# Kernel tuning notes

Measured on AMD Instinct MI355X. Metric: run time of the kernel, lower is better.

The kernel has to match this reference:

```python
import jax, jax.numpy as jnp
import numpy as np

HIDDEN = 4096
N_HEADS = 32
N_KV_HEADS = 2
HEAD_DIM = 128          # hidden // n_heads
ROT_DIM = HEAD_DIM // 2  # partial rotary (ChatGLM style)
ROPE_THETA = 10000.0
Q_SIZE = N_HEADS * HEAD_DIM
KV_SIZE = N_KV_HEADS * HEAD_DIM
SCALE = HEAD_DIM ** -0.5
T = 2048


def setup_inputs() -> dict:
    key = jax.random.key(0)
    k1, k2, k3, k4 = jax.random.split(key, 4)
    hidden_states = jax.random.normal(k1, (T, HIDDEN), dtype=jnp.float32)
    positions = jnp.arange(T, dtype=jnp.int64) if jax.config.jax_enable_x64 else jnp.arange(T, dtype=jnp.int32)
    w_qkv = jax.random.normal(k2, (Q_SIZE + 2 * KV_SIZE, HIDDEN), dtype=jnp.float32) * 0.02
    b_qkv = jax.random.normal(k3, (Q_SIZE + 2 * KV_SIZE,), dtype=jnp.float32) * 0.02
    w_dense = jax.random.normal(k4, (HIDDEN, Q_SIZE), dtype=jnp.float32) * 0.02
    return {"hidden_states": hidden_states, "positions": positions,
            "w_qkv": w_qkv, "b_qkv": b_qkv, "w_dense": w_dense}


def _apply_rope(x, positions):
    # x: [T, H, HEAD_DIM]; interleaved (is_neox_style=False) partial rotary on first ROT_DIM dims
    half = ROT_DIM // 2
    inv_freq = 1.0 / (ROPE_THETA ** (jnp.arange(0, half, dtype=jnp.float32) * 2.0 / ROT_DIM))
    freqs = positions.astype(jnp.float32)[:, None] * inv_freq[None, :]   # [T, half]
    cos = jnp.cos(freqs)[:, None, :]  # [T, 1, half]
    sin = jnp.sin(freqs)[:, None, :]
    x_rot = x[..., :ROT_DIM]
    x_pass = x[..., ROT_DIM:]
    x1 = x_rot[..., 0::2]
    x2 = x_rot[..., 1::2]
    o1 = x1 * cos - x2 * sin
    o2 = x2 * cos + x1 * sin
    rot = jnp.stack([o1, o2], axis=-1).reshape(x_rot.shape)  # re-interleave
    return jnp.concatenate([rot, x_pass], axis=-1)


def reference(hidden_states, positions, w_qkv, b_qkv, w_dense):
    # QKV projection (bias from add_qkv_bias=True)
    qkv = hidden_states @ w_qkv.T + b_qkv                     # [T, 4608]
    q = qkv[:, :Q_SIZE].reshape(T, N_HEADS, HEAD_DIM)
    k = qkv[:, Q_SIZE:Q_SIZE + KV_SIZE].reshape(T, N_KV_HEADS, HEAD_DIM)
    v = qkv[:, Q_SIZE + KV_SIZE:].reshape(T, N_KV_HEADS, HEAD_DIM)

    q = _apply_rope(q, positions)
    k = _apply_rope(k, positions)

    # GQA: expand 2 kv heads -> 32 q heads (each kv head serves 16 q heads)
    rep = N_HEADS // N_KV_HEADS
    k = jnp.repeat(k, rep, axis=1)                            # [T, 32, 128]
    v = jnp.repeat(v, rep, axis=1)

    # Causal scaled dot-product attention
    scores = jnp.einsum('thd,shd->hts', q, k) * SCALE         # [H, T, T]
    causal = positions[:, None] >= positions[None, :]          # [T, T]
    scores = jnp.where(causal[None, :, :], scores, jnp.finfo(scores.dtype).min)
    probs = jax.nn.softmax(scores, axis=-1)
    attn = jnp.einsum('hts,shd->thd', probs, v).reshape(T, Q_SIZE)

    # Output projection (no bias: add_bias_linear=False)
    return attn @ w_dense.T
```

## Files before the change

### kernel.cpp

```cpp
#include <hip/hip_runtime.h>
#include <cstdint>
#include <math.h>

typedef __bf16 bf16;
typedef __bf16 bf16x8 __attribute__((ext_vector_type(8)));
typedef __bf16 bf16x4 __attribute__((ext_vector_type(4)));
typedef float f32x4 __attribute__((ext_vector_type(4)));

#define T_SEQ 2048
#define HID   4096
#define NQH   32
#define NKVH  2
#define HD    128
#define NQKV  4608
#define ATT_SCALE 0.08838834764831845f

__device__ __forceinline__ void load_lds16(const void* g, void* l) {
    auto gp = (const __attribute__((address_space(1))) unsigned int*)(uintptr_t)g;
    auto lp = (__attribute__((address_space(3))) unsigned int*)(unsigned int)(uintptr_t)l;
    __builtin_amdgcn_global_load_lds(gp, lp, 16, 0, 0);
}

__device__ __forceinline__ f32x4 mfma16(bf16x8 a, bf16x8 b, f32x4 c) {
    return __builtin_amdgcn_mfma_f32_16x16x32_bf16(a, b, c, 0, 0, 0);
}

__global__ void cvt_f32_bf16_kernel(const float* __restrict__ x, bf16* __restrict__ y) {
    size_t i = ((size_t)blockIdx.x * 256 + threadIdx.x) * 8;
    float4 a = *(const float4*)(x + i);
    float4 b = *(const float4*)(x + i + 4);
    bf16x8 o;
    o[0] = (bf16)a.x; o[1] = (bf16)a.y; o[2] = (bf16)a.z; o[3] = (bf16)a.w;
    o[4] = (bf16)b.x; o[5] = (bf16)b.y; o[6] = (bf16)b.z; o[7] = (bf16)b.w;
    *(bf16x8*)(y + i) = o;
}

template <int OUT_BF16, int HAS_BIAS>
__global__ __launch_bounds__(256) void gemm_bt(const bf16* __restrict__ A,
                                               const bf16* __restrict__ B,
                                               const float* __restrict__ bias,
                                               void* __restrict__ Cout,
                                               int M, int N, int K) {
    __shared__ __align__(16) char sA[16384];
    __shared__ __align__(16) char sB[16384];
    const int tid = threadIdx.x;
    const int wid = tid >> 6, l = tid & 63, l4 = l >> 4, l16 = l & 15;
    const int wm = wid >> 1, wn = wid & 1;
    const int bm = blockIdx.x * 128, bn = blockIdx.y * 128;

    f32x4 acc[4][4] = {};

    const int c = tid;
    const int row0 = c >> 3, cc0 = c & 7;

    for (int k0 = 0; k0 < K; k0 += 64) {
        __syncthreads();
#pragma unroll
        for (int c4 = 0; c4 < 4; ++c4) {
            int ch = c4 * 256 + tid;
            int row = ch >> 3, cch = ch & 7;
            int scc = cch ^ (row & 7);
            load_lds16(A + (size_t)(bm + row) * K + k0 + scc * 8,
                       sA + c4 * 4096 + wid * 1024);
        }
#pragma unroll
        for (int c4 = 0; c4 < 4; ++c4) {
            int ch = c4 * 256 + tid;
            int row = ch >> 3, cch = ch & 7;
            int scc = cch ^ (row & 7);
            load_lds16(B + (size_t)(bn + row) * K + k0 + scc * 8,
                       sB + c4 * 4096 + wid * 1024);
        }
        __syncthreads();
#pragma unroll
        for (int ks = 0; ks < 2; ++ks) {
            bf16x8 af[4], bfr[4];
#pragma unroll
            for (int mi = 0; mi < 4; ++mi) {
                int row = wm * 64 + mi * 16 + l16;
                af[mi] = *(const bf16x8*)(sA + row * 128 + ((ks * 64 + l4 * 16) ^ ((row & 7) << 4)));
            }
#pragma unroll
            for (int ni = 0; ni < 4; ++ni) {
                int row = wn * 64 + ni * 16 + l16;
                bfr[ni] = *(const bf16x8*)(sB + row * 128 + ((ks * 64 + l4 * 16) ^ ((row & 7) << 4)));
            }
#pragma unroll
            for (int mi = 0; mi < 4; ++mi)
#pragma unroll
                for (int ni = 0; ni < 4; ++ni)
                    acc[mi][ni] = mfma16(af[mi], bfr[ni], acc[mi][ni]);
        }
    }
    (void)row0; (void)cc0;

#pragma unroll
    for (int mi = 0; mi < 4; ++mi)
#pragma unroll
        for (int ni = 0; ni < 4; ++ni) {
            const int col = bn + wn * 64 + ni * 16 + l16;
            float bv = HAS_BIAS ? bias[col] : 0.0f;
#pragma unroll
            for (int r = 0; r < 4; ++r) {
                const int row = bm + wm * 64 + mi * 16 + l4 * 4 + r;
                float val = acc[mi][ni][r] + bv;
                if (OUT_BF16)
                    ((bf16*)Cout)[(size_t)row * N + col] = (bf16)val;
                else
                    ((float*)Cout)[(size_t)row * N + col] = val;
            }
        }
}

__global__ void rope_qk_kernel(const bf16* __restrict__ qkv,
                               bf16* __restrict__ qheads, bf16* __restrict__ kheads) {
    const int t = blockIdx.x;
    const int g = blockIdx.y;
    const int sub = threadIdx.x >> 6;
    const int l = threadIdx.x & 63;
    const bf16* src;
    bf16* dst;
    if (g < 8) {
        int hh = g * 4 + sub;
        src = qkv + (size_t)t * NQKV + hh * HD;
        dst = qheads + ((size_t)hh * T_SEQ + t) * HD;
    } else {
        if (sub >= 2) return;
        src = qkv + (size_t)t * NQKV + HID + sub * HD;
        dst = kheads + ((size_t)sub * T_SEQ + t) * HD;
    }
    if (l < 32) {
        const int i = l;
        float x1 = (float)src[2 * i], x2 = (float)src[2 * i + 1];
        float fr = (float)t * exp2f((float)i * (-13.287712379549449f / 32.0f));
        float sn = sinf(fr), cs = cosf(fr);
        dst[2 * i] = (bf16)(x1 * cs - x2 * sn);
        dst[2 * i + 1] = (bf16)(x2 * cs + x1 * sn);
    } else {
        const int j = l - 32;
        dst[64 + 2 * j] = src[64 + 2 * j];
        dst[64 + 2 * j + 1] = src[64 + 2 * j + 1];
    }
}

__global__ void v_trans_kernel(const bf16* __restrict__ qkv, bf16* __restrict__ vt) {
    const int c = threadIdx.x;
    const int kvh = c >> 7, d = c & 127;
    const int t0 = blockIdx.x * 8;
#pragma unroll
    for (int i = 0; i < 8; ++i) {
        int t = t0 + i;
        vt[((size_t)kvh * HD + d) * T_SEQ + t] = qkv[(size_t)t * NQKV + 4352 + c];
    }
}

__global__ __launch_bounds__(256) void attn_fwd_kernel(const bf16* __restrict__ qh,
                                                       const bf16* __restrict__ kh,
                                                       const bf16* __restrict__ vt,
                                                       bf16* __restrict__ attnb) {
    __shared__ __align__(16) char sK[16384];
    __shared__ __align__(16) char sV[16384];
    __shared__ __align__(16) char sP[4][2048];
    const int tid = threadIdx.x;
    const int wid = tid >> 6, l = tid & 63, l4 = l >> 4, l16 = l & 15;
    const int qt = blockIdx.x, h = blockIdx.y, kvh = h >> 4;

    bf16x8 qf[4];
    {
        const bf16* qb = qh + ((size_t)h * T_SEQ + qt * 64 + wid * 16 + l16) * HD + l4 * 8;
#pragma unroll
        for (int f = 0; f < 4; ++f) qf[f] = *(const bf16x8*)(qb + f * 32);
    }
    f32x4 o[8] = {};
    float mr[4], lr[4];
#pragma unroll
    for (int r = 0; r < 4; ++r) { mr[r] = -INFINITY; lr[r] = 0.f; }

    for (int kt = 0; kt <= qt; ++kt) {
        __syncthreads();
#pragma unroll
        for (int c4 = 0; c4 < 4; ++c4) {
            int c = c4 * 256 + tid;
            int row = c >> 4, cc = c & 15;
            int scc = cc ^ (row & 7);
            load_lds16(kh + ((size_t)kvh * T_SEQ + kt * 64 + row) * HD + scc * 8,
                       sK + c4 * 4096 + wid * 1024);
        }
#pragma unroll
        for (int c4 = 0; c4 < 4; ++c4) {
            int c = c4 * 256 + tid;
            int row = c >> 3, cc = c & 7;
            int scc = cc ^ (row & 7);
            load_lds16(vt + ((size_t)kvh * HD + row) * T_SEQ + kt * 64 + scc * 8,
                       sV + c4 * 4096 + wid * 1024);
        }
        __syncthreads();

        f32x4 s[4] = {};
#pragma unroll
        for (int ct = 0; ct < 4; ++ct)
#pragma unroll
            for (int ks = 0; ks < 4; ++ks) {
                int row = ct * 16 + l16;
                bf16x8 kf = *(const bf16x8*)(sK + row * 256 + ((ks * 64 + l4 * 16) ^ ((row & 7) << 4)));
                s[ct] = mfma16(qf[ks], kf, s[ct]);
            }

        const bool diag = (kt == qt);
        float sv[4][4];
#pragma unroll
        for (int ct = 0; ct < 4; ++ct)
#pragma unroll
            for (int r = 0; r < 4; ++r) {
                float x = s[ct][r] * ATT_SCALE;
                if (diag && (ct * 16 + l16) > (wid * 16 + l4 * 4 + r)) x = -INFINITY;
                sv[ct][r] = x;
            }

#pragma unroll
        for (int r = 0; r < 4; ++r) {
            float mx = fmaxf(fmaxf(sv[0][r], sv[1][r]), fmaxf(sv[2][r], sv[3][r]));
            mx = fmaxf(mx, __shfl_xor(mx, 1));
            mx = fmaxf(mx, __shfl_xor(mx, 2));
            mx = fmaxf(mx, __shfl_xor(mx, 4));
            mx = fmaxf(mx, __shfl_xor(mx, 8));
            float mn = fmaxf(mr[r], mx);
            float al = __expf(mr[r] - mn);
            mr[r] = mn;
            float p[4], ps = 0.f;
#pragma unroll
            for (int ct = 0; ct < 4; ++ct) { p[ct] = __expf(sv[ct][r] - mn); ps += p[ct]; }
            ps += __shfl_xor(ps, 1);
            ps += __shfl_xor(ps, 2);
            ps += __shfl_xor(ps, 4);
            ps += __shfl_xor(ps, 8);
            lr[r] = lr[r] * al + ps;
            const int prow = l4 * 4 + r;
#pragma unroll
            for (int ct = 0; ct < 4; ++ct)
                *(bf16*)(sP[wid] + prow * 128 + (((ct * 16 + l16) * 2) ^ ((prow & 7) << 4))) = (bf16)p[ct];
#pragma unroll
            for (int nt = 0; nt < 8; ++nt) o[nt][r] *= al;
        }

#pragma unroll
        for (int ks = 0; ks < 2; ++ks) {
            bf16x8 pa = *(const bf16x8*)(sP[wid] + l16 * 128 + ((ks * 64 + l4 * 16) ^ ((l16 & 7) << 4)));
#pragma unroll
            for (int nt = 0; nt < 8; ++nt) {
                int vrow = nt * 16 + l16;
                bf16x8 vf = *(const bf16x8*)(sV + vrow * 128 + ((ks * 64 + l4 * 16) ^ ((vrow & 7) << 4)));
                o[nt] = mfma16(pa, vf, o[nt]);
            }
        }
    }

    float inv[4];
#pragma unroll
    for (int r = 0; r < 4; ++r) inv[r] = 1.0f / lr[r];
#pragma unroll
    for (int nt = 0; nt < 8; ++nt)
#pragma unroll
        for (int r = 0; r < 4; ++r) {
            int row = qt * 64 + wid * 16 + l4 * 4 + r;
            int col = h * HD + nt * 16 + l16;
            attnb[(size_t)row * HID + col] = (bf16)(o[nt][r] * inv[r]);
        }
}

extern "C" void kernel_launch(void* const* d_in, const int* in_sizes, int n_in,
                              void* d_out, int out_size, void* d_ws, size_t ws_size,
                              hipStream_t stream) {
    const float* hs = (const float*)d_in[0];
    const float* wqkv = (const float*)d_in[2];
    const float* bqkv = (const float*)d_in[3];
    const float* wdense = (const float*)d_in[4];
    float* out = (float*)d_out;

    char* ws = (char*)d_ws;
    bf16* wqkvb   = (bf16*)(ws + 0);
    bf16* hb      = (bf16*)(ws + 37748736);
    bf16* qkvb    = (bf16*)(ws + 54525952);
    bf16* qhp     = (bf16*)(ws + 0);
    bf16* khp     = (bf16*)(ws + 16777216);
    bf16* vtp     = (bf16*)(ws + 17825792);
    bf16* wdenseb = (bf16*)(ws + 18874368);
    bf16* attnb   = (bf16*)(ws + 54525952);
    (void)in_sizes; (void)n_in; (void)out_size; (void)ws_size;

    cvt_f32_bf16_kernel<<<(T_SEQ * HID) / 2048, 256, 0, stream>>>(hs, hb);
    cvt_f32_bf16_kernel<<<(NQKV * HID) / 2048, 256, 0, stream>>>(wqkv, wqkvb);

    dim3 g1(T_SEQ / 128, NQKV / 128);
    gemm_bt<1, 1><<<g1, 256, 0, stream>>>(hb, wqkvb, bqkv, (void*)qkvb, T_SEQ, NQKV, HID);

    cvt_f32_bf16_kernel<<<(HID * HID) / 2048, 256, 0, stream>>>(wdense, wdenseb);

    rope_qk_kernel<<<dim3(T_SEQ, 9), 256, 0, stream>>>(qkvb, qhp, khp);
    v_trans_kernel<<<T_SEQ / 8, 256, 0, stream>>>(qkvb, vtp);

    attn_fwd_kernel<<<dim3(T_SEQ / 64, NQH), 256, 0, stream>>>(qhp, khp, vtp, attnb);

    dim3 g2(T_SEQ / 128, HID / 128);
    gemm_bt<0, 0><<<g2, 256, 0, stream>>>(attnb, wdenseb, nullptr, (void*)out, T_SEQ, HID, HID);
}
```

Measured before the change: 398.7 us.

## Restructure attention with paired causal tiles, double-buffered KV, lazy rescale

```diff
diff --git a/kernel.cpp b/kernel.cpp
--- a/kernel.cpp
+++ b/kernel.cpp
@@ -50,9 +50,6 @@
 
     f32x4 acc[4][4] = {};
 
-    const int c = tid;
-    const int row0 = c >> 3, cc0 = c & 7;
-
     for (int k0 = 0; k0 < K; k0 += 64) {
         __syncthreads();
 #pragma unroll
@@ -92,7 +89,6 @@
                     acc[mi][ni] = mfma16(af[mi], bfr[ni], acc[mi][ni]);
         }
     }
-    (void)row0; (void)cc0;
 
 #pragma unroll
     for (int mi = 0; mi < 4; ++mi)
@@ -154,118 +150,150 @@
     }
 }
 
-__global__ __launch_bounds__(256) void attn_fwd_kernel(const bf16* __restrict__ qh,
-                                                       const bf16* __restrict__ kh,
-                                                       const bf16* __restrict__ vt,
-                                                       bf16* __restrict__ attnb) {
-    __shared__ __align__(16) char sK[16384];
-    __shared__ __align__(16) char sV[16384];
-    __shared__ __align__(16) char sP[4][2048];
+__global__ __launch_bounds__(128, 1) void attn_fwd_kernel(const bf16* __restrict__ qh,
+                                                          const bf16* __restrict__ kh,
+                                                          const bf16* __restrict__ vt,
+                                                          bf16* __restrict__ attnb) {
+    __shared__ __align__(16) char sK[2][16384];
+    __shared__ __align__(16) char sV[2][16384];
+    __shared__ __align__(16) char sP[2][4096];
     const int tid = threadIdx.x;
     const int wid = tid >> 6, l = tid & 63, l4 = l >> 4, l16 = l & 15;
-    const int qt = blockIdx.x, h = blockIdx.y, kvh = h >> 4;
-
-    bf16x8 qf[4];
-    {
-        const bf16* qb = qh + ((size_t)h * T_SEQ + qt * 64 + wid * 16 + l16) * HD + l4 * 8;
-#pragma unroll
-        for (int f = 0; f < 4; ++f) qf[f] = *(const bf16x8*)(qb + f * 32);
-    }
-    f32x4 o[8] = {};
-    float mr[4], lr[4];
-#pragma unroll
-    for (int r = 0; r < 4; ++r) { mr[r] = -INFINITY; lr[r] = 0.f; }
-
-    for (int kt = 0; kt <= qt; ++kt) {
+    const int pair = blockIdx.x, h = blockIdx.y, kvh = h >> 4;
+
+    auto stageKV = [&](int buf, int kt) {
+#pragma unroll
+        for (int c4 = 0; c4 < 8; ++c4) {
+            int ch = c4 * 128 + tid;
+            int row = ch >> 4, cc = ch & 15;
+            load_lds16(kh + ((size_t)kvh * T_SEQ + kt * 64 + row) * HD + (cc ^ (row & 7)) * 8,
+                       sK[buf] + c4 * 2048 + wid * 1024);
+        }
+#pragma unroll
+        for (int c4 = 0; c4 < 8; ++c4) {
+            int ch = c4 * 128 + tid;
+            int row = ch >> 3, cc = ch & 7;
+            load_lds16(vt + ((size_t)kvh * HD + row) * T_SEQ + kt * 64 + (cc ^ (row & 7)) * 8,
+                       sV[buf] + c4 * 2048 + wid * 1024);
+        }
+    };
+
+    auto process = [&](int qb) {
+        bf16x8 qf[2][4];
+#pragma unroll
+        for (int rg = 0; rg < 2; ++rg) {
+            const bf16* qp = qh + ((size_t)h * T_SEQ + qb * 64 + wid * 32 + rg * 16 + l16) * HD + l4 * 8;
+#pragma unroll
+            for (int f = 0; f < 4; ++f) qf[rg][f] = *(const bf16x8*)(qp + f * 32);
+        }
+        f32x4 o[2][8] = {};
+        float mr[2][4], lr[2][4];
+#pragma unroll
+        for (int rg = 0; rg < 2; ++rg)
+#pragma unroll
+            for (int r = 0; r < 4; ++r) { mr[rg][r] = -INFINITY; lr[rg][r] = 0.f; }
+
+        const int nt = qb + 1;
+        stageKV(0, 0);
         __syncthreads();
-#pragma unroll
-        for (int c4 = 0; c4 < 4; ++c4) {
-            int c = c4 * 256 + tid;
-            int row = c >> 4, cc = c & 15;
-            int scc = cc ^ (row & 7);
-            load_lds16(kh + ((size_t)kvh * T_SEQ + kt * 64 + row) * HD + scc * 8,
-                       sK + c4 * 4096 + wid * 1024);
-        }
-#pragma unroll
-        for (int c4 = 0; c4 < 4; ++c4) {
-            int c = c4 * 256 + tid;
-            int row = c >> 3, cc = c & 7;
-            int scc = cc ^ (row & 7);
-            load_lds16(vt + ((size_t)kvh * HD + row) * T_SEQ + kt * 64 + scc * 8,
-                       sV + c4 * 4096 + wid * 1024);
-        }
-        __syncthreads();
-
-        f32x4 s[4] = {};
-#pragma unroll
-        for (int ct = 0; ct < 4; ++ct)
-#pragma unroll
-            for (int ks = 0; ks < 4; ++ks) {
-                int row = ct * 16 + l16;
-                bf16x8 kf = *(const bf16x8*)(sK + row * 256 + ((ks * 64 + l4 * 16) ^ ((row & 7) << 4)));
-                s[ct] = mfma16(qf[ks], kf, s[ct]);
-            }
-
-        const bool diag = (kt == qt);
-        float sv[4][4];
-#pragma unroll
-        for (int ct = 0; ct < 4; ++ct)
+        int cur = 0;
+        for (int kt = 0; kt < nt; ++kt) {
+            if (kt + 1 < nt) stageKV(cur ^ 1, kt + 1);
+
+            f32x4 s[2][4] = {};
+#pragma unroll
+            for (int ct = 0; ct < 4; ++ct)
+#pragma unroll
+                for (int ks = 0; ks < 4; ++ks) {
+                    int row = ct * 16 + l16;
+                    bf16x8 kf = *(const bf16x8*)(sK[cur] + row * 256 + ((ks * 64 + l4 * 16) ^ ((row & 7) << 4)));
+                    s[0][ct] = mfma16(qf[0][ks], kf, s[0][ct]);
+                    s[1][ct] = mfma16(qf[1][ks], kf, s[1][ct]);
+                }
+
+            const bool diag = (kt == qb);
+            float sv[2][4][4];
+#pragma unroll
+            for (int rg = 0; rg < 2; ++rg)
+#pragma unroll
+                for (int ct = 0; ct < 4; ++ct)
+#pragma unroll
+                    for (int r = 0; r < 4; ++r) {
+                        float x = s[rg][ct][r] * ATT_SCALE;
+                        if (diag && (ct * 16 + l16) > (wid * 32 + rg * 16 + l4 * 4 + r)) x = -INFINITY;
+                        sv[rg][ct][r] = x;
+                    }
+
+#pragma unroll
+            for (int rg = 0; rg < 2; ++rg)
+#pragma unroll
+                for (int r = 0; r < 4; ++r) {
+                    float mx = fmaxf(fmaxf(sv[rg][0][r], sv[rg][1][r]), fmaxf(sv[rg][2][r], sv[rg][3][r]));
+                    mx = fmaxf(mx, __shfl_xor(mx, 1));
+                    mx = fmaxf(mx, __shfl_xor(mx, 2));
+                    mx = fmaxf(mx, __shfl_xor(mx, 4));
+                    mx = fmaxf(mx, __shfl_xor(mx, 8));
+                    if (!__all(mx <= mr[rg][r] + 8.0f)) {
+                        float mn = fmaxf(mr[rg][r], mx);
+                        float al = __expf(mr[rg][r] - mn);
+                        mr[rg][r] = mn;
+                        lr[rg][r] *= al;
+#pragma unroll
+                        for (int n2 = 0; n2 < 8; ++n2) o[rg][n2][r] *= al;
+                    }
+                    float ps = 0.f;
+                    const int prow = rg * 16 + l4 * 4 + r;
+#pragma unroll
+                    for (int ct = 0; ct < 4; ++ct) {
+                        float p = __expf(sv[rg][ct][r] - mr[rg][r]);
+                        ps += p;
+                        *(bf16*)(sP[wid] + prow * 128 + (((ct * 16 + l16) * 2) ^ ((prow & 7) << 4))) = (bf16)p;
+                    }
+                    lr[rg][r] += ps;
+                }
+
+#pragma unroll
+            for (int ks = 0; ks < 2; ++ks) {
+                bf16x8 pa0 = *(const bf16x8*)(sP[wid] + l16 * 128 + ((ks * 64 + l4 * 16) ^ ((l16 & 7) << 4)));
+                bf16x8 pa1 = *(const bf16x8*)(sP[wid] + (16 + l16) * 128 + ((ks * 64 + l4 * 16) ^ ((l16 & 7) << 4)));
+#pragma unroll
+                for (int n2 = 0; n2 < 8; ++n2) {
+                    int vrow = n2 * 16 + l16;
+                    bf16x8 vf = *(const bf16x8*)(sV[cur] + vrow * 128 + ((ks * 64 + l4 * 16) ^ ((vrow & 7) << 4)));
+                    o[0][n2] = mfma16(pa0, vf, o[0][n2]);
+                    o[1][n2] = mfma16(pa1, vf, o[1][n2]);
+                }
+            }
+            __syncthreads();
+            cur ^= 1;
+        }
+
+        float inv[2][4];
+#pragma unroll
+        for (int rg = 0; rg < 2; ++rg)
 #pragma unroll
             for (int r = 0; r < 4; ++r) {
-                float x = s[ct][r] * ATT_SCALE;
-                if (diag && (ct * 16 + l16) > (wid * 16 + l4 * 4 + r)) x = -INFINITY;
-                sv[ct][r] = x;
-            }
-
-#pragma unroll
-        for (int r = 0; r < 4; ++r) {
-            float mx = fmaxf(fmaxf(sv[0][r], sv[1][r]), fmaxf(sv[2][r], sv[3][r]));
-            mx = fmaxf(mx, __shfl_xor(mx, 1));
-            mx = fmaxf(mx, __shfl_xor(mx, 2));
-            mx = fmaxf(mx, __shfl_xor(mx, 4));
-            mx = fmaxf(mx, __shfl_xor(mx, 8));
-            float mn = fmaxf(mr[r], mx);
-            float al = __expf(mr[r] - mn);
-            mr[r] = mn;
-            float p[4], ps = 0.f;
-#pragma unroll
-            for (int ct = 0; ct < 4; ++ct) { p[ct] = __expf(sv[ct][r] - mn); ps += p[ct]; }
-            ps += __shfl_xor(ps, 1);
-            ps += __shfl_xor(ps, 2);
-            ps += __shfl_xor(ps, 4);
-            ps += __shfl_xor(ps, 8);
-            lr[r] = lr[r] * al + ps;
-            const int prow = l4 * 4 + r;
-#pragma unroll
-            for (int ct = 0; ct < 4; ++ct)
-                *(bf16*)(sP[wid] + prow * 128 + (((ct * 16 + l16) * 2) ^ ((prow & 7) << 4))) = (bf16)p[ct];
-#pragma unroll
-            for (int nt = 0; nt < 8; ++nt) o[nt][r] *= al;
-        }
-
-#pragma unroll
-        for (int ks = 0; ks < 2; ++ks) {
-            bf16x8 pa = *(const bf16x8*)(sP[wid] + l16 * 128 + ((ks * 64 + l4 * 16) ^ ((l16 & 7) << 4)));
-#pragma unroll
-            for (int nt = 0; nt < 8; ++nt) {
-                int vrow = nt * 16 + l16;
-                bf16x8 vf = *(const bf16x8*)(sV + vrow * 128 + ((ks * 64 + l4 * 16) ^ ((vrow & 7) << 4)));
-                o[nt] = mfma16(pa, vf, o[nt]);
-            }
-        }
-    }
-
-    float inv[4];
-#pragma unroll
-    for (int r = 0; r < 4; ++r) inv[r] = 1.0f / lr[r];
-#pragma unroll
-    for (int nt = 0; nt < 8; ++nt)
-#pragma unroll
-        for (int r = 0; r < 4; ++r) {
-            int row = qt * 64 + wid * 16 + l4 * 4 + r;
-            int col = h * HD + nt * 16 + l16;
-            attnb[(size_t)row * HID + col] = (bf16)(o[nt][r] * inv[r]);
-        }
+                float s2 = lr[rg][r];
+                s2 += __shfl_xor(s2, 1);
+                s2 += __shfl_xor(s2, 2);
+                s2 += __shfl_xor(s2, 4);
+                s2 += __shfl_xor(s2, 8);
+                inv[rg][r] = 1.0f / s2;
+            }
+#pragma unroll
+        for (int rg = 0; rg < 2; ++rg)
+#pragma unroll
+            for (int n2 = 0; n2 < 8; ++n2)
+#pragma unroll
+                for (int r = 0; r < 4; ++r) {
+                    int row = qb * 64 + wid * 32 + rg * 16 + l4 * 4 + r;
+                    int col = h * HD + n2 * 16 + l16;
+                    attnb[(size_t)row * HID + col] = (bf16)(o[rg][n2][r] * inv[rg][r]);
+                }
+    };
+
+    process(pair);
+    process(31 - pair);
 }
 
 extern "C" void kernel_launch(void* const* d_in, const int* in_sizes, int n_in,
@@ -299,7 +327,7 @@
     rope_qk_kernel<<<dim3(T_SEQ, 9), 256, 0, stream>>>(qkvb, qhp, khp);
     v_trans_kernel<<<T_SEQ / 8, 256, 0, stream>>>(qkvb, vtp);
 
-    attn_fwd_kernel<<<dim3(T_SEQ / 64, NQH), 256, 0, stream>>>(qhp, khp, vtp, attnb);
+    attn_fwd_kernel<<<dim3(16, NQH), 128, 0, stream>>>(qhp, khp, vtp, attnb);
 
     dim3 g2(T_SEQ / 128, HID / 128);
     gemm_bt<0, 0><<<g2, 256, 0, stream>>>(attnb, wdenseb, nullptr, (void*)out, T_SEQ, HID, HID);
```

Result: faster. 354.0 us (-11.2%).
